# Kernel optimization log

Hardware: AMD Instinct MI355X
Metric: run time of the kernel (lower is better)

The kernel has to match this reference:

```python
import jax, jax.numpy as jnp
import numpy as np
from jax.scipy.special import logsumexp

VOCAB, EMB, HID, K = 50000, 256, 512, 48
H = HID // 2
B, T = 64, 512


def setup_inputs() -> dict:
    key = jax.random.key(0)
    ks = jax.random.split(key, 15)
    f = lambda k, s: jax.random.normal(k, s, jnp.float32) * 0.1
    return {
        "x": jax.random.randint(ks[0], (B, T), 0, VOCAB),
        "tags": jax.random.randint(ks[1], (B, T), 0, K),
        "mask": jnp.ones((B, T), jnp.bool_),
        "emb": f(ks[2], (VOCAB, EMB)),
        "Wih_f": f(ks[3], (4 * H, EMB)),
        "Whh_f": f(ks[4], (4 * H, H)),
        "b_f": f(ks[5], (4 * H,)),
        "Wih_b": f(ks[6], (4 * H, EMB)),
        "Whh_b": f(ks[7], (4 * H, H)),
        "b_b": f(ks[8], (4 * H,)),
        "fc_W": f(ks[9], (K, HID)),
        "fc_b": f(ks[10], (K,)),
        "start_t": f(ks[11], (K,)),
        "end_t": f(ks[12], (K,)),
        "trans": f(ks[13], (K, K)),
    }


def _lstm_dir(xs, Wih, Whh, b, reverse):
    # xs: [S, N, E]; scan over axis 0 (PyTorch gate order i,f,g,o; bias = b_ih+b_hh)
    n = xs.shape[1]
    hdim = Whh.shape[1]

    def step(carry, x_t):
        h, c = carry
        gates = x_t @ Wih.T + h @ Whh.T + b
        i, fg, g, o = jnp.split(gates, 4, axis=-1)
        i = jax.nn.sigmoid(i)
        fg = jax.nn.sigmoid(fg)
        g = jnp.tanh(g)
        o = jax.nn.sigmoid(o)
        c = fg * c + i * g
        h = o * jnp.tanh(c)
        return (h, c), h

    init = (jnp.zeros((n, hdim), xs.dtype), jnp.zeros((n, hdim), xs.dtype))
    _, hs = jax.lax.scan(step, init, xs, reverse=reverse)
    return hs


def _crf_nll(emissions, tags, mask, start_t, end_t, trans):
    # torchcrf with batch_first=True, reduction='mean'; returns -llh.mean()
    em = jnp.transpose(emissions, (1, 0, 2))  # [T,B,K] time-major
    tg = tags.T                                # [T,B]
    m = mask.T.astype(em.dtype)                # [T,B]
    bidx = jnp.arange(em.shape[1])

    # numerator: score of the gold tag path
    emit = jnp.take_along_axis(em, tg[..., None], axis=-1)[..., 0]  # [T,B]
    tr = trans[tg[:-1], tg[1:]]                                      # [T-1,B]
    num = start_t[tg[0]] + emit[0] + jnp.sum((tr + emit[1:]) * m[1:], axis=0)
    last = (jnp.sum(mask, axis=1) - 1).astype(jnp.int32)             # [B]
    num = num + end_t[tg[last, bidx]]

    # denominator: forward algorithm (sequential logsumexp recurrence)
    def step(alpha, inp):
        e_t, m_t = inp
        nxt = logsumexp(alpha[:, :, None] + trans[None] + e_t[:, None, :], axis=1)
        return jnp.where(m_t[:, None] > 0, nxt, alpha), None

    alpha0 = start_t + em[0]                     # [B,K]
    alpha, _ = jax.lax.scan(step, alpha0, (em[1:], m[1:]))
    den = logsumexp(alpha + end_t, axis=-1)      # [B]
    return -jnp.mean(num - den)


def reference(x, tags, mask, emb, Wih_f, Whh_f, b_f, Wih_b, Whh_b, b_b, fc_W, fc_b, start_t, end_t, trans):
    table = emb.at[0].set(0.0)  # padding_idx=0 row is zero
    e = table[x]                # [B,T,EMB]
    # Faithful to source: batch-first embeds fed into a seq-first nn.LSTM,
    # so the recurrence runs over axis 0 (the data batch axis).
    h_f = _lstm_dir(e, Wih_f, Whh_f, b_f, False)
    h_b = _lstm_dir(e, Wih_b, Whh_b, b_b, True)
    lstm_out = jnp.concatenate([h_f, h_b], axis=-1)  # [B,T,HID]
    emissions = lstm_out @ fc_W.T + fc_b             # [B,T,K]
    return _crf_nll(emissions, tags, mask, start_t, end_t, trans)
```

## Files before the change

### kernel.cpp

```cpp
#include <hip/hip_runtime.h>
#include <hip/hip_bf16.h>

#define VOCAB 50000
#define EMBD 256
#define HIDD 512
#define KTAG 48
#define HD 256
#define BB 64
#define TT 512
#define GATES 1024

typedef __bf16 bf16x8 __attribute__((ext_vector_type(8)));
typedef float f32x4 __attribute__((ext_vector_type(4)));

#define GLDS16(gp, lp) __builtin_amdgcn_global_load_lds( \
    (const __attribute__((address_space(1))) void*)(gp), \
    (__attribute__((address_space(3))) void*)(lp), 16, 0, 0)

__device__ __forceinline__ f32x4 mfma16(bf16x8 a, bf16x8 b, f32x4 c){
  return __builtin_amdgcn_mfma_f32_16x16x32_bf16(a, b, c, 0, 0, 0);
}
__device__ __forceinline__ float fsig(float x){
  return __builtin_amdgcn_rcpf(1.0f + __expf(-x));
}
__device__ __forceinline__ float ftanh(float x){
  x = fminf(10.0f, fmaxf(-10.0f, x));
  float e = __expf(2.0f*x);
  return (e - 1.0f) * __builtin_amdgcn_rcpf(e + 1.0f);
}

__global__ __launch_bounds__(256) void convert_all(
    const float* emb, const float* wf, const float* wb,
    const float* uf, const float* ub, const float* fc,
    __bf16* o_emb, __bf16* o_wih, __bf16* o_uf, __bf16* o_ub, __bf16* o_fc){
  const long N_emb = (long)VOCAB*EMBD;
  const long N_w   = 1024L*256;
  const long N_fc  = 48L*512;
  const long total = N_emb + 4*N_w + N_fc;
  for (long i = (long)blockIdx.x*256 + threadIdx.x; i < total; i += (long)gridDim.x*256){
    long j = i;
    if (j < N_emb){ o_emb[j] = (__bf16)((j < EMBD) ? 0.0f : emb[j]); continue; }
    j -= N_emb;
    if (j < N_w){ o_wih[j] = (__bf16)wf[j]; continue; }
    j -= N_w;
    if (j < N_w){ o_wih[N_w + j] = (__bf16)wb[j]; continue; }
    j -= N_w;
    if (j < N_w){ o_uf[j] = (__bf16)uf[j]; continue; }
    j -= N_w;
    if (j < N_w){ o_ub[j] = (__bf16)ub[j]; continue; }
    j -= N_w;
    o_fc[j] = (__bf16)fc[j];
  }
}

__global__ __launch_bounds__(256) void gemm_pre(const int* x, const __bf16* embb,
                                                const __bf16* wih, __bf16* pre){
  __shared__ __attribute__((aligned(16))) __bf16 As[128*32];
  __shared__ __attribute__((aligned(16))) __bf16 Bs[128*32];
  const int bid = blockIdx.x;
  const int bm = bid >> 4, bn = bid & 15;
  const int m0 = bm*128, n0 = bn*128;
  const int tid = threadIdx.x, l = tid & 63, w = tid >> 6;
  const int lr = l & 15, lk = l >> 4;
  const int wm = w >> 1, wn = w & 1;
  f32x4 acc[4][4];
  #pragma unroll
  for (int a=0;a<4;a++) for (int b2=0;b2<4;b2++) acc[a][b2] = (f32x4){0.f,0.f,0.f,0.f};

  const __bf16* agp[2];
  const __bf16* bgp[2];
  #pragma unroll
  for (int c=0;c<2;c++){
    const int id = w*2 + c;
    const int slot = id*64 + l;
    const int r = slot >> 2, kk = (slot & 3)*8;
    const int idx = x[m0 + r];
    agp[c] = embb + (size_t)idx*EMBD + kk;
    bgp[c] = wih + (size_t)(n0 + r)*EMBD + kk;
  }

  for (int k0 = 0; k0 < EMBD; k0 += 32){
    __syncthreads();
    #pragma unroll
    for (int c=0;c<2;c++){
      const int id = w*2 + c;
      GLDS16(agp[c] + k0, As + id*512);
      GLDS16(bgp[c] + k0, Bs + id*512);
    }
    asm volatile("s_waitcnt vmcnt(0)" ::: "memory");
    __syncthreads();
    bf16x8 af[4], bfr[4];
    #pragma unroll
    for (int mt=0;mt<4;mt++) af[mt] = *(const bf16x8*)(&As[(wm*64 + mt*16 + lr)*32 + lk*8]);
    #pragma unroll
    for (int nt=0;nt<4;nt++) bfr[nt] = *(const bf16x8*)(&Bs[(wn*64 + nt*16 + lr)*32 + lk*8]);
    #pragma unroll
    for (int mt=0;mt<4;mt++)
      #pragma unroll
      for (int nt=0;nt<4;nt++)
        acc[mt][nt] = mfma16(af[mt], bfr[nt], acc[mt][nt]);
  }
  #pragma unroll
  for (int mt=0;mt<4;mt++)
    #pragma unroll
    for (int nt=0;nt<4;nt++)
      #pragma unroll
      for (int r=0;r<4;r++){
        const int row = m0 + wm*64 + mt*16 + lk*4 + r;
        const int col = n0 + wn*64 + nt*16 + lr;
        pre[(size_t)row*2048 + col] = (__bf16)acc[mt][nt][r];
      }
}

__global__ __launch_bounds__(512, 1) void lstm_rec(const __bf16* pre, const __bf16* whhF,
                                                   const __bf16* whhB, const float* biasF,
                                                   const float* biasB, __bf16* hcat){
  __shared__ __attribute__((aligned(16))) __bf16 hLDS[16*264];
  __shared__ __attribute__((aligned(16))) __bf16 preLDS[2][16*1032];
  const int bid = blockIdx.x;
  const int dir = bid & 1, tg = bid >> 1;
  const int t0 = tg*16;
  const int tid = threadIdx.x, l = tid & 63, w = tid >> 6;
  const int lr = l & 15, lk = l >> 4;
  const __bf16* whh = dir ? whhB : whhF;
  const float* bias = dir ? biasB : biasF;

  bf16x8 Bf[4][2][8];
  #pragma unroll
  for (int q=0;q<4;q++)
    #pragma unroll
    for (int j=0;j<2;j++)
      #pragma unroll
      for (int kt=0;kt<8;kt++){
        const int n = q*256 + w*32 + j*16 + lr;
        Bf[q][j][kt] = *(const bf16x8*)(&whh[(size_t)n*HD + kt*32 + lk*8]);
      }

  float brg[4][2];
  #pragma unroll
  for (int q=0;q<4;q++)
    #pragma unroll
    for (int j=0;j<2;j++)
      brg[q][j] = bias[q*256 + w*32 + j*16 + lr];

  float cst[2][4];
  #pragma unroll
  for (int j=0;j<2;j++)
    #pragma unroll
    for (int r=0;r<4;r++) cst[j][r] = 0.f;

  auto stage = [&](int buf, int bs){
    #pragma unroll
    for (int c2=0;c2<4;c2++){
      const int id = w*4 + c2;
      const int r = id >> 1, half = id & 1;
      const __bf16* g = pre + (size_t)(bs*TT + t0 + r)*2048 + dir*1024 + half*512 + l*8;
      GLDS16(g, &preLDS[buf][r*1032 + half*512]);
    }
  };

  stage(0, dir ? (BB-1) : 0);
  int prev_b = 0;

  #pragma unroll 1
  for (int s = 0; s < BB; s++){
    const int bs = dir ? (BB-1 - s) : s;
    const int buf = s & 1;
    asm volatile("s_waitcnt vmcnt(0)" ::: "memory");
    __syncthreads();
    if (s < BB-1) stage(buf^1, dir ? (BB-2 - s) : (s+1));
    if (s > 0){
      const int row = tid >> 5, ch = tid & 31;
      bf16x8 hv = *(const bf16x8*)(&hLDS[row*264 + ch*8]);
      *(bf16x8*)(&hcat[(size_t)(prev_b*TT + t0 + row)*HIDD + dir*HD + ch*8]) = hv;
    }
    f32x4 acc[4][2];
    #pragma unroll
    for (int q=0;q<4;q++)
      #pragma unroll
      for (int j=0;j<2;j++) acc[q][j] = (f32x4){0.f,0.f,0.f,0.f};
    if (s > 0){
      #pragma unroll
      for (int kt=0; kt<8; kt++){
        bf16x8 a = *(const bf16x8*)(&hLDS[lr*264 + kt*32 + lk*8]);
        #pragma unroll
        for (int q=0;q<4;q++)
          #pragma unroll
          for (int j=0;j<2;j++)
            acc[q][j] = mfma16(a, Bf[q][j][kt], acc[q][j]);
      }
    }
    __syncthreads();
    #pragma unroll
    for (int j=0;j<2;j++){
      const int colbase = w*32 + j*16 + lr;
      #pragma unroll
      for (int r=0;r<4;r++){
        const int row = lk*4 + r;
        float gi = acc[0][j][r] + (float)preLDS[buf][row*1032 +       colbase] + brg[0][j];
        float gf = acc[1][j][r] + (float)preLDS[buf][row*1032 + 256 + colbase] + brg[1][j];
        float gg = acc[2][j][r] + (float)preLDS[buf][row*1032 + 512 + colbase] + brg[2][j];
        float go = acc[3][j][r] + (float)preLDS[buf][row*1032 + 768 + colbase] + brg[3][j];
        float iv = fsig(gi), fv = fsig(gf), gv = ftanh(gg), ov = fsig(go);
        float cn = fv*cst[j][r] + iv*gv;
        cst[j][r] = cn;
        hLDS[row*264 + colbase] = (__bf16)(ov * ftanh(cn));
      }
    }
    prev_b = bs;
  }
  __syncthreads();
  {
    const int row = tid >> 5, ch = tid & 31;
    bf16x8 hv = *(const bf16x8*)(&hLDS[row*264 + ch*8]);
    *(bf16x8*)(&hcat[(size_t)(prev_b*TT + t0 + row)*HIDD + dir*HD + ch*8]) = hv;
  }
}

__global__ __launch_bounds__(256) void gemm_emis(const __bf16* hcat, const __bf16* fcw,
                                                 const float* fcb, float* emis){
  const int tid = threadIdx.x, l = tid & 63, w = tid >> 6;
  const int lr = l & 15, lk = l >> 4;
  const size_t m0 = (size_t)blockIdx.x*64 + w*16;
  f32x4 acc[3];
  #pragma unroll
  for (int nt=0;nt<3;nt++) acc[nt] = (f32x4){0.f,0.f,0.f,0.f};
  #pragma unroll
  for (int kt=0; kt<16; kt++){
    bf16x8 a = *(const bf16x8*)(&hcat[(m0 + lr)*HIDD + kt*32 + lk*8]);
    #pragma unroll
    for (int nt=0;nt<3;nt++){
      bf16x8 b = *(const bf16x8*)(&fcw[(size_t)(nt*16 + lr)*HIDD + kt*32 + lk*8]);
      acc[nt] = mfma16(a, b, acc[nt]);
    }
  }
  #pragma unroll
  for (int nt=0;nt<3;nt++){
    const int col = nt*16 + lr;
    const float bv = fcb[col];
    #pragma unroll
    for (int r=0;r<4;r++){
      const size_t row = m0 + lk*4 + r;
      emis[row*KTAG + col] = acc[nt][r] + bv;
    }
  }
}

__global__ __launch_bounds__(64) void crf_num(const int* tags, const float* emis,
                                              const float* trans, const float* start_t,
                                              const float* end_t, float* numv){
  const int b = blockIdx.x, l = threadIdx.x;
  float part = 0.f;
  for (int t = l; t < TT; t += 64){
    const int tg = tags[b*TT + t];
    const float e = emis[(size_t)(b*TT + t)*KTAG + tg];
    if (t > 0){
      const int tp = tags[b*TT + t - 1];
      part += trans[tp*KTAG + tg] + e;
    } else {
      part += start_t[tg] + e;
    }
  }
  #pragma unroll
  for (int off=32; off; off >>= 1) part += __shfl_down(part, off);
  if (l == 0){
    const int tl = tags[b*TT + TT - 1];
    numv[b] = part + end_t[tl];
  }
}

__global__ __launch_bounds__(64) void crf_den(const float* emis, const float* trans,
                                              const float* start_t, const float* end_t,
                                              float* denv){
  __shared__ float wlds[64];
  const int b = blockIdx.x, l = threadIdx.x;
  float E[48];
  #pragma unroll
  for (int j=0;j<48;j++) E[j] = (l < KTAG) ? __expf(trans[j*KTAG + l]) : 0.f;
  float alpha = (l < KTAG) ? (start_t[l] + emis[(size_t)(b*TT)*KTAG + l]) : -1e30f;

  float em_cur = (l < KTAG) ? emis[(size_t)(b*TT + 1)*KTAG + l] : 0.f;
  #pragma unroll 1
  for (int t = 1; t < TT; t++){
    float em_nxt = (l < KTAG && t < TT-1) ? emis[(size_t)(b*TT + t + 1)*KTAG + l] : 0.f;
    float m = alpha;
    #pragma unroll
    for (int off=32; off; off >>= 1) m = fmaxf(m, __shfl_xor(m, off));
    const float wv = __expf(alpha - m);
    wlds[l] = wv;
    asm volatile("s_waitcnt lgkmcnt(0)" ::: "memory");
    float s = 0.f;
    #pragma unroll
    for (int j=0;j<48;j+=4){
      const float4 w4 = *(const float4*)(&wlds[j]);
      s += w4.x*E[j] + w4.y*E[j+1] + w4.z*E[j+2] + w4.w*E[j+3];
    }
    asm volatile("" ::: "memory");
    alpha = (l < KTAG) ? (em_cur + m + __logf(s)) : -1e30f;
    em_cur = em_nxt;
  }
  float v = (l < KTAG) ? (alpha + end_t[l]) : -1e30f;
  float mf = v;
  #pragma unroll
  for (int off=32; off; off >>= 1) mf = fmaxf(mf, __shfl_xor(mf, off));
  float sv = __expf(v - mf);
  #pragma unroll
  for (int off=32; off; off >>= 1) sv += __shfl_xor(sv, off);
  if (l == 0) denv[b] = mf + __logf(sv);
}

__global__ __launch_bounds__(64) void finalize(const float* numv, const float* denv, float* out){
  const int l = threadIdx.x;
  float v = numv[l] - denv[l];
  #pragma unroll
  for (int off=32; off; off >>= 1) v += __shfl_down(v, off);
  if (l == 0) out[0] = -v * (1.0f/64.0f);
}

extern "C" void kernel_launch(void* const* d_in, const int* in_sizes, int n_in,
                              void* d_out, int out_size, void* d_ws, size_t ws_size,
                              hipStream_t stream){
  const int*   x     = (const int*)d_in[0];
  const int*   tags  = (const int*)d_in[1];
  const float* emb   = (const float*)d_in[3];
  const float* wih_f = (const float*)d_in[4];
  const float* whh_f = (const float*)d_in[5];
  const float* b_f   = (const float*)d_in[6];
  const float* wih_b = (const float*)d_in[7];
  const float* whh_b = (const float*)d_in[8];
  const float* b_b   = (const float*)d_in[9];
  const float* fc_W  = (const float*)d_in[10];
  const float* fc_b  = (const float*)d_in[11];
  const float* start_t = (const float*)d_in[12];
  const float* end_t   = (const float*)d_in[13];
  const float* trans   = (const float*)d_in[14];

  constexpr size_t SZ_EMBB = (size_t)VOCAB*EMBD*2;
  constexpr size_t SZ_WIH  = (size_t)2048*256*2;
  constexpr size_t SZ_WHH  = (size_t)1024*256*2;
  constexpr size_t SZ_FCW  = (size_t)48*512*2;
  constexpr size_t SZ_PRE  = (size_t)32768*2048*2;
  constexpr size_t SZ_HCAT = (size_t)32768*512*2;
  constexpr size_t SZ_EMIS = (size_t)32768*48*4;
  constexpr size_t TOTAL = SZ_EMBB + SZ_WIH + 2*SZ_WHH + SZ_FCW + SZ_PRE + SZ_HCAT + SZ_EMIS + 512;
  if (ws_size < TOTAL){ hipMemsetAsync(d_out, 0, sizeof(float), stream); return; }

  char* ws = (char*)d_ws;
  size_t off = 0;
  __bf16* embb  = (__bf16*)(ws + off); off += SZ_EMBB;
  __bf16* wihb  = (__bf16*)(ws + off); off += SZ_WIH;
  __bf16* whhfb = (__bf16*)(ws + off); off += SZ_WHH;
  __bf16* whhbb = (__bf16*)(ws + off); off += SZ_WHH;
  __bf16* fcwb  = (__bf16*)(ws + off); off += SZ_FCW;
  __bf16* pre   = (__bf16*)(ws + off); off += SZ_PRE;
  __bf16* hcat  = (__bf16*)(ws + off); off += SZ_HCAT;
  float*  emis  = (float*)(ws + off);  off += SZ_EMIS;
  float*  numv  = (float*)(ws + off);  off += 256;
  float*  denv  = (float*)(ws + off);

  convert_all<<<4096, 256, 0, stream>>>(emb, wih_f, wih_b, whh_f, whh_b, fc_W,
                                        embb, wihb, whhfb, whhbb, fcwb);
  gemm_pre<<<4096, 256, 0, stream>>>(x, embb, wihb, pre);
  lstm_rec<<<64, 512, 0, stream>>>(pre, whhfb, whhbb, b_f, b_b, hcat);
  gemm_emis<<<512, 256, 0, stream>>>(hcat, fcwb, fc_b, emis);
  crf_num<<<64, 64, 0, stream>>>(tags, emis, trans, start_t, end_t, numv);
  crf_den<<<64, 64, 0, stream>>>(emis, trans, start_t, end_t, denv);
  finalize<<<1, 64, 0, stream>>>(numv, denv, (float*)d_out);
}
```

Before: 1.005 ms.

## Stream recurrent weights from cache each step instead of holding them in registers

```diff
diff --git a/kernel.cpp b/kernel.cpp
--- a/kernel.cpp
+++ b/kernel.cpp
@@ -54,7 +54,8 @@
 }
 
 __global__ __launch_bounds__(256) void gemm_pre(const int* x, const __bf16* embb,
-                                                const __bf16* wih, __bf16* pre){
+                                                const __bf16* wih, const float* bf,
+                                                const float* bb2, __bf16* pre){
   __shared__ __attribute__((aligned(16))) __bf16 As[128*32];
   __shared__ __attribute__((aligned(16))) __bf16 Bs[128*32];
   const int bid = blockIdx.x;
@@ -103,18 +104,19 @@
   #pragma unroll
   for (int mt=0;mt<4;mt++)
     #pragma unroll
-    for (int nt=0;nt<4;nt++)
+    for (int nt=0;nt<4;nt++){
+      const int col = n0 + wn*64 + nt*16 + lr;
+      const float bv = (col < GATES) ? bf[col] : bb2[col - GATES];
       #pragma unroll
       for (int r=0;r<4;r++){
         const int row = m0 + wm*64 + mt*16 + lk*4 + r;
-        const int col = n0 + wn*64 + nt*16 + lr;
-        pre[(size_t)row*2048 + col] = (__bf16)acc[mt][nt][r];
-      }
-}
-
-__global__ __launch_bounds__(512, 1) void lstm_rec(const __bf16* pre, const __bf16* whhF,
-                                                   const __bf16* whhB, const float* biasF,
-                                                   const float* biasB, __bf16* hcat){
+        pre[(size_t)row*2048 + col] = (__bf16)(acc[mt][nt][r] + bv);
+      }
+    }
+}
+
+__global__ __launch_bounds__(512, 2) void lstm_rec(const __bf16* pre, const __bf16* whhF,
+                                                   const __bf16* whhB, __bf16* hcat){
   __shared__ __attribute__((aligned(16))) __bf16 hLDS[16*264];
   __shared__ __attribute__((aligned(16))) __bf16 preLDS[2][16*1032];
   const int bid = blockIdx.x;
@@ -123,25 +125,8 @@
   const int tid = threadIdx.x, l = tid & 63, w = tid >> 6;
   const int lr = l & 15, lk = l >> 4;
   const __bf16* whh = dir ? whhB : whhF;
-  const float* bias = dir ? biasB : biasF;
-
-  bf16x8 Bf[4][2][8];
-  #pragma unroll
-  for (int q=0;q<4;q++)
-    #pragma unroll
-    for (int j=0;j<2;j++)
-      #pragma unroll
-      for (int kt=0;kt<8;kt++){
-        const int n = q*256 + w*32 + j*16 + lr;
-        Bf[q][j][kt] = *(const bf16x8*)(&whh[(size_t)n*HD + kt*32 + lk*8]);
-      }
-
-  float brg[4][2];
-  #pragma unroll
-  for (int q=0;q<4;q++)
-    #pragma unroll
-    for (int j=0;j<2;j++)
-      brg[q][j] = bias[q*256 + w*32 + j*16 + lr];
+
+  const __bf16* wbase = whh + (size_t)(w*32 + lr)*HD + lk*8;
 
   float cst[2][4];
   #pragma unroll
@@ -168,43 +153,82 @@
     const int buf = s & 1;
     asm volatile("s_waitcnt vmcnt(0)" ::: "memory");
     __syncthreads();
-    if (s < BB-1) stage(buf^1, dir ? (BB-2 - s) : (s+1));
+
     if (s > 0){
-      const int row = tid >> 5, ch = tid & 31;
-      bf16x8 hv = *(const bf16x8*)(&hLDS[row*264 + ch*8]);
-      *(bf16x8*)(&hcat[(size_t)(prev_b*TT + t0 + row)*HIDD + dir*HD + ch*8]) = hv;
-    }
-    f32x4 acc[4][2];
-    #pragma unroll
-    for (int q=0;q<4;q++)
-      #pragma unroll
-      for (int j=0;j<2;j++) acc[q][j] = (f32x4){0.f,0.f,0.f,0.f};
-    if (s > 0){
-      #pragma unroll
-      for (int kt=0; kt<8; kt++){
-        bf16x8 a = *(const bf16x8*)(&hLDS[lr*264 + kt*32 + lk*8]);
+      bf16x8 bufA[16], bufB[16];
+      #pragma unroll
+      for (int f=0; f<16; f++){
+        bufA[f] = *(const bf16x8*)(wbase +         (f>>3)*4096 + (f&7)*32);
+        bufB[f] = *(const bf16x8*)(wbase + 65536 + (f>>3)*4096 + (f&7)*32);
+      }
+      {
+        const int row = tid >> 5, ch = tid & 31;
+        bf16x8 hv = *(const bf16x8*)(&hLDS[row*264 + ch*8]);
+        *(bf16x8*)(&hcat[(size_t)(prev_b*TT + t0 + row)*HIDD + dir*HD + ch*8]) = hv;
+      }
+      bf16x8 af[8];
+      #pragma unroll
+      for (int kt=0; kt<8; kt++) af[kt] = *(const bf16x8*)(&hLDS[lr*264 + kt*32 + lk*8]);
+
+      f32x4 acc[4][2];
+      #pragma unroll
+      for (int q=0;q<4;q++)
         #pragma unroll
-        for (int q=0;q<4;q++)
-          #pragma unroll
-          for (int j=0;j<2;j++)
-            acc[q][j] = mfma16(a, Bf[q][j][kt], acc[q][j]);
-      }
-    }
-    __syncthreads();
-    #pragma unroll
-    for (int j=0;j<2;j++){
-      const int colbase = w*32 + j*16 + lr;
-      #pragma unroll
-      for (int r=0;r<4;r++){
-        const int row = lk*4 + r;
-        float gi = acc[0][j][r] + (float)preLDS[buf][row*1032 +       colbase] + brg[0][j];
-        float gf = acc[1][j][r] + (float)preLDS[buf][row*1032 + 256 + colbase] + brg[1][j];
-        float gg = acc[2][j][r] + (float)preLDS[buf][row*1032 + 512 + colbase] + brg[2][j];
-        float go = acc[3][j][r] + (float)preLDS[buf][row*1032 + 768 + colbase] + brg[3][j];
-        float iv = fsig(gi), fv = fsig(gf), gv = ftanh(gg), ov = fsig(go);
-        float cn = fv*cst[j][r] + iv*gv;
-        cst[j][r] = cn;
-        hLDS[row*264 + colbase] = (__bf16)(ov * ftanh(cn));
+        for (int j=0;j<2;j++) acc[q][j] = (f32x4){0.f,0.f,0.f,0.f};
+
+      #pragma unroll
+      for (int f=0; f<16; f++) acc[0][f>>3] = mfma16(af[f&7], bufA[f], acc[0][f>>3]);
+      __builtin_amdgcn_sched_barrier(0);
+      #pragma unroll
+      for (int f=0; f<16; f++)
+        bufA[f] = *(const bf16x8*)(wbase + 2*65536 + (f>>3)*4096 + (f&7)*32);
+      #pragma unroll
+      for (int f=0; f<16; f++) acc[1][f>>3] = mfma16(af[f&7], bufB[f], acc[1][f>>3]);
+      __builtin_amdgcn_sched_barrier(0);
+      #pragma unroll
+      for (int f=0; f<16; f++)
+        bufB[f] = *(const bf16x8*)(wbase + 3*65536 + (f>>3)*4096 + (f&7)*32);
+      if (s < BB-1) stage(buf^1, dir ? (BB-2 - s) : (s+1));
+      #pragma unroll
+      for (int f=0; f<16; f++) acc[2][f>>3] = mfma16(af[f&7], bufA[f], acc[2][f>>3]);
+      #pragma unroll
+      for (int f=0; f<16; f++) acc[3][f>>3] = mfma16(af[f&7], bufB[f], acc[3][f>>3]);
+
+      __syncthreads();
+      #pragma unroll
+      for (int j=0;j<2;j++){
+        const int colbase = w*32 + j*16 + lr;
+        #pragma unroll
+        for (int r=0;r<4;r++){
+          const int row = lk*4 + r;
+          float gi = acc[0][j][r] + (float)preLDS[buf][row*1032 +       colbase];
+          float gf = acc[1][j][r] + (float)preLDS[buf][row*1032 + 256 + colbase];
+          float gg = acc[2][j][r] + (float)preLDS[buf][row*1032 + 512 + colbase];
+          float go = acc[3][j][r] + (float)preLDS[buf][row*1032 + 768 + colbase];
+          float iv = fsig(gi), fv = fsig(gf), gv = ftanh(gg), ov = fsig(go);
+          float cn = fv*cst[j][r] + iv*gv;
+          cst[j][r] = cn;
+          hLDS[row*264 + colbase] = (__bf16)(ov * ftanh(cn));
+        }
+      }
+    } else {
+      if (s < BB-1) stage(buf^1, dir ? (BB-2 - s) : (s+1));
+      __syncthreads();
+      #pragma unroll
+      for (int j=0;j<2;j++){
+        const int colbase = w*32 + j*16 + lr;
+        #pragma unroll
+        for (int r=0;r<4;r++){
+          const int row = lk*4 + r;
+          float gi = (float)preLDS[buf][row*1032 +       colbase];
+          float gf = (float)preLDS[buf][row*1032 + 256 + colbase];
+          float gg = (float)preLDS[buf][row*1032 + 512 + colbase];
+          float go = (float)preLDS[buf][row*1032 + 768 + colbase];
+          float iv = fsig(gi), fv = fsig(gf), gv = ftanh(gg), ov = fsig(go);
+          float cn = fv*cst[j][r] + iv*gv;
+          cst[j][r] = cn;
+          hLDS[row*264 + colbase] = (__bf16)(ov * ftanh(cn));
+        }
       }
     }
     prev_b = bs;
@@ -360,8 +384,8 @@
 
   convert_all<<<4096, 256, 0, stream>>>(emb, wih_f, wih_b, whh_f, whh_b, fc_W,
                                         embb, wihb, whhfb, whhbb, fcwb);
-  gemm_pre<<<4096, 256, 0, stream>>>(x, embb, wihb, pre);
-  lstm_rec<<<64, 512, 0, stream>>>(pre, whhfb, whhbb, b_f, b_b, hcat);
+  gemm_pre<<<4096, 256, 0, stream>>>(x, embb, wihb, b_f, b_b, pre);
+  lstm_rec<<<64, 512, 0, stream>>>(pre, whhfb, whhbb, hcat);
   gemm_emis<<<512, 256, 0, stream>>>(hcat, fcwb, fc_b, emis);
   crf_num<<<64, 64, 0, stream>>>(tags, emis, trans, start_t, end_t, numv);
   crf_den<<<64, 64, 0, stream>>>(emis, trans, start_t, end_t, denv);
```

New measurement: 1.556 ms. 54.9% more time.
